# Optimization experiments

Hardware: AMD Instinct MI355X
Metric: run time of the kernel (lower is better)

Reference implementation:

```python
import jax, jax.numpy as jnp
import numpy as np

ECHO_SCALE = 22.8


def setup_inputs() -> dict:
    key = jax.random.key(0)
    k1, k2, k3, k4 = jax.random.split(key, 4)
    n, m = 8192, 4096
    y = jax.random.normal(k1, (n, m), dtype=jnp.float32)
    y_echo = jax.random.normal(k2, (n, m), dtype=jnp.float32)
    f = jax.random.normal(k3, (n, m), dtype=jnp.float32)
    mu = jax.random.uniform(k4, (1,), dtype=jnp.float32)  # scalar threshold in (0,1)
    return {"y": y, "y_echo": y_echo, "f": f, "mu": mu}


def reference(y, y_echo, f, mu):
    n = y.shape[0]
    abs_y = jnp.abs(y)
    # pseudo_l0: hard indicator for |y| >= mu, linear ramp |y|/mu for 0 < |y| < mu
    # (torch precedence: (|y|>=mu) + ((0<|y|<mu) / mu * |y|))
    hard = (abs_y >= mu).astype(y.dtype)
    soft = jnp.logical_and(abs_y > 0, abs_y < mu).astype(y.dtype) / mu * abs_y
    pseudo_l0_loss = jnp.sum(hard + soft) / n
    # l2: trace(|diff| @ |diff|^T) == sum(|diff|**2); same math, no [n,n] matmul
    diff = y_echo / ECHO_SCALE - f
    l2_loss = jnp.sum(jnp.abs(diff) ** 2) / n
    return (pseudo_l0_loss, l2_loss)
```

## Files before the change

### kernel.cpp

```cpp
#include <hip/hip_runtime.h>


#define ECHO_SCALE 22.8f
#define N_ROWS 8192.0f

typedef float fx4 __attribute__((ext_vector_type(4)));

__global__ void init_out_kernel(float* out) {
    if (threadIdx.x < 2) out[threadIdx.x] = 0.0f;
}

__device__ __forceinline__ fx4 ldnt(const fx4* p) {
    return __builtin_nontemporal_load(p);
}

__device__ __forceinline__ void consume(const fx4& vy, const fx4& ve,
                                        const fx4& vf, float inv_mu,
                                        float inv_echo, float& s0, float& s1) {
    s0 += fminf(fabsf(vy.x) * inv_mu, 1.0f);
    s0 += fminf(fabsf(vy.y) * inv_mu, 1.0f);
    s0 += fminf(fabsf(vy.z) * inv_mu, 1.0f);
    s0 += fminf(fabsf(vy.w) * inv_mu, 1.0f);
    float dx = ve.x * inv_echo - vf.x;
    float dy = ve.y * inv_echo - vf.y;
    float dz = ve.z * inv_echo - vf.z;
    float dw = ve.w * inv_echo - vf.w;
    s1 += dx * dx;
    s1 += dy * dy;
    s1 += dz * dz;
    s1 += dw * dw;
}

__global__ __launch_bounds__(256) void loss_kernel(
    const fx4* __restrict__ y,
    const fx4* __restrict__ ye,
    const fx4* __restrict__ f,
    const float* __restrict__ mu_ptr,
    float* __restrict__ out,
    long long n4)
{
    const float mu = mu_ptr[0];
    const float inv_mu = 1.0f / mu;
    const float inv_echo = 1.0f / ECHO_SCALE;

    float s0a = 0.0f, s0b = 0.0f;
    float s1a = 0.0f, s1b = 0.0f;

    const long long per_block = (n4 + gridDim.x - 1) / gridDim.x;
    const long long start = (long long)blockIdx.x * per_block;
    long long end = start + per_block;
    if (end > n4) end = n4;

    const int tid = threadIdx.x;
    const long long bs = blockDim.x;

    long long i = start + tid;
    for (; i + bs < end; i += 2 * bs) {
        fx4 vy0 = ldnt(&y[i]);
        fx4 vy1 = ldnt(&y[i + bs]);
        fx4 ve0 = ldnt(&ye[i]);
        fx4 ve1 = ldnt(&ye[i + bs]);
        fx4 vf0 = ldnt(&f[i]);
        fx4 vf1 = ldnt(&f[i + bs]);
        consume(vy0, ve0, vf0, inv_mu, inv_echo, s0a, s1a);
        consume(vy1, ve1, vf1, inv_mu, inv_echo, s0b, s1b);
    }
    for (; i < end; i += bs) {
        fx4 vy = ldnt(&y[i]);
        fx4 ve = ldnt(&ye[i]);
        fx4 vf = ldnt(&f[i]);
        consume(vy, ve, vf, inv_mu, inv_echo, s0a, s1a);
    }

    float s0 = s0a + s0b;
    float s1 = s1a + s1b;

    #pragma unroll
    for (int off = 32; off > 0; off >>= 1) {
        s0 += __shfl_down(s0, off, 64);
        s1 += __shfl_down(s1, off, 64);
    }

    __shared__ float l0[4];
    __shared__ float l1[4];
    const int wave = threadIdx.x >> 6;
    const int lane = threadIdx.x & 63;
    if (lane == 0) { l0[wave] = s0; l1[wave] = s1; }
    __syncthreads();

    if (threadIdx.x == 0) {
        float t0 = 0.0f, t1 = 0.0f;
        #pragma unroll
        for (int w = 0; w < 4; ++w) { t0 += l0[w]; t1 += l1[w]; }
        atomicAdd(&out[0], t0 * (1.0f / N_ROWS));
        atomicAdd(&out[1], t1 * (1.0f / N_ROWS));
    }
}

extern "C" void kernel_launch(void* const* d_in, const int* in_sizes, int n_in,
                              void* d_out, int out_size, void* d_ws, size_t ws_size,
                              hipStream_t stream) {
    const fx4* y  = (const fx4*)d_in[0];
    const fx4* ye = (const fx4*)d_in[1];
    const fx4* f  = (const fx4*)d_in[2];
    const float* mu  = (const float*)d_in[3];
    float* out = (float*)d_out;

    const long long n  = (long long)in_sizes[0];
    const long long n4 = n / 4;

    init_out_kernel<<<1, 64, 0, stream>>>(out);

    const int block = 256;
    int grid = 2048;
    long long needed = (n4 + block - 1) / block;
    if (needed < grid) grid = (int)needed;

    loss_kernel<<<grid, block, 0, stream>>>(y, ye, f, mu, out, n4);
}
```

Before: 92.77 us.

## Split loss reduction into separate y and echo/f block groups

```diff
diff --git a/kernel.cpp b/kernel.cpp
--- a/kernel.cpp
+++ b/kernel.cpp
@@ -3,6 +3,8 @@
 
 #define ECHO_SCALE 22.8f
 #define N_ROWS 8192.0f
+#define NY_BLOCKS 1024
+#define NEF_BLOCKS 2048
 
 typedef float fx4 __attribute__((ext_vector_type(4)));
 
@@ -14,24 +16,22 @@
     return __builtin_nontemporal_load(p);
 }
 
-__device__ __forceinline__ void consume(const fx4& vy, const fx4& ve,
-                                        const fx4& vf, float inv_mu,
-                                        float inv_echo, float& s0, float& s1) {
-    s0 += fminf(fabsf(vy.x) * inv_mu, 1.0f);
-    s0 += fminf(fabsf(vy.y) * inv_mu, 1.0f);
-    s0 += fminf(fabsf(vy.z) * inv_mu, 1.0f);
-    s0 += fminf(fabsf(vy.w) * inv_mu, 1.0f);
-    float dx = ve.x * inv_echo - vf.x;
-    float dy = ve.y * inv_echo - vf.y;
-    float dz = ve.z * inv_echo - vf.z;
-    float dw = ve.w * inv_echo - vf.w;
-    s1 += dx * dx;
-    s1 += dy * dy;
-    s1 += dz * dz;
-    s1 += dw * dw;
+__device__ __forceinline__ float pl0_4(const fx4& v, float inv_mu) {
+    return fminf(fabsf(v.x) * inv_mu, 1.0f)
+         + fminf(fabsf(v.y) * inv_mu, 1.0f)
+         + fminf(fabsf(v.z) * inv_mu, 1.0f)
+         + fminf(fabsf(v.w) * inv_mu, 1.0f);
 }
 
-__global__ __launch_bounds__(256) void loss_kernel(
+__device__ __forceinline__ float l2_4(const fx4& e, const fx4& ff, float inv_echo) {
+    float dx = e.x * inv_echo - ff.x;
+    float dy = e.y * inv_echo - ff.y;
+    float dz = e.z * inv_echo - ff.z;
+    float dw = e.w * inv_echo - ff.w;
+    return dx * dx + dy * dy + dz * dz + dw * dw;
+}
+
+__global__ __launch_bounds__(256) void loss_split_kernel(
     const fx4* __restrict__ y,
     const fx4* __restrict__ ye,
     const fx4* __restrict__ f,
@@ -39,61 +39,65 @@
     float* __restrict__ out,
     long long n4)
 {
-    const float mu = mu_ptr[0];
-    const float inv_mu = 1.0f / mu;
-    const float inv_echo = 1.0f / ECHO_SCALE;
+    __shared__ float lred[4];
+    const int bid = blockIdx.x;
+    const int tid = threadIdx.x;
+    const long long bs = 256;
 
-    float s0a = 0.0f, s0b = 0.0f;
-    float s1a = 0.0f, s1b = 0.0f;
+    float s = 0.0f;
+    int out_idx;
 
-    const long long per_block = (n4 + gridDim.x - 1) / gridDim.x;
-    const long long start = (long long)blockIdx.x * per_block;
-    long long end = start + per_block;
-    if (end > n4) end = n4;
+    if (bid < NY_BLOCKS) {
+        out_idx = 0;
+        const float inv_mu = 1.0f / mu_ptr[0];
+        const long long pb = (n4 + NY_BLOCKS - 1) / NY_BLOCKS;
+        const long long start = (long long)bid * pb;
+        long long end = start + pb; if (end > n4) end = n4;
 
-    const int tid = threadIdx.x;
-    const long long bs = blockDim.x;
+        float sa = 0.0f, sb = 0.0f;
+        long long i = start + tid;
+        for (; i + bs < end; i += 2 * bs) {
+            fx4 v0 = ldnt(&y[i]);
+            fx4 v1 = ldnt(&y[i + bs]);
+            sa += pl0_4(v0, inv_mu);
+            sb += pl0_4(v1, inv_mu);
+        }
+        for (; i < end; i += bs) sa += pl0_4(ldnt(&y[i]), inv_mu);
+        s = sa + sb;
+    } else {
+        out_idx = 1;
+        const float inv_echo = 1.0f / ECHO_SCALE;
+        const int eb = bid - NY_BLOCKS;
+        const long long pb = (n4 + NEF_BLOCKS - 1) / NEF_BLOCKS;
+        const long long start = (long long)eb * pb;
+        long long end = start + pb; if (end > n4) end = n4;
 
-    long long i = start + tid;
-    for (; i + bs < end; i += 2 * bs) {
-        fx4 vy0 = ldnt(&y[i]);
-        fx4 vy1 = ldnt(&y[i + bs]);
-        fx4 ve0 = ldnt(&ye[i]);
-        fx4 ve1 = ldnt(&ye[i + bs]);
-        fx4 vf0 = ldnt(&f[i]);
-        fx4 vf1 = ldnt(&f[i + bs]);
-        consume(vy0, ve0, vf0, inv_mu, inv_echo, s0a, s1a);
-        consume(vy1, ve1, vf1, inv_mu, inv_echo, s0b, s1b);
-    }
-    for (; i < end; i += bs) {
-        fx4 vy = ldnt(&y[i]);
-        fx4 ve = ldnt(&ye[i]);
-        fx4 vf = ldnt(&f[i]);
-        consume(vy, ve, vf, inv_mu, inv_echo, s0a, s1a);
+        float sa = 0.0f, sb = 0.0f;
+        long long i = start + tid;
+        for (; i + bs < end; i += 2 * bs) {
+            fx4 e0 = ldnt(&ye[i]);
+            fx4 e1 = ldnt(&ye[i + bs]);
+            fx4 f0 = ldnt(&f[i]);
+            fx4 f1 = ldnt(&f[i + bs]);
+            sa += l2_4(e0, f0, inv_echo);
+            sb += l2_4(e1, f1, inv_echo);
+        }
+        for (; i < end; i += bs) sa += l2_4(ldnt(&ye[i]), ldnt(&f[i]), inv_echo);
+        s = sa + sb;
     }
 
-    float s0 = s0a + s0b;
-    float s1 = s1a + s1b;
+    #pragma unroll
+    for (int off = 32; off > 0; off >>= 1)
+        s += __shfl_down(s, off, 64);
 
-    #pragma unroll
-    for (int off = 32; off > 0; off >>= 1) {
-        s0 += __shfl_down(s0, off, 64);
-        s1 += __shfl_down(s1, off, 64);
-    }
-
-    __shared__ float l0[4];
-    __shared__ float l1[4];
-    const int wave = threadIdx.x >> 6;
-    const int lane = threadIdx.x & 63;
-    if (lane == 0) { l0[wave] = s0; l1[wave] = s1; }
+    const int wave = tid >> 6;
+    const int lane = tid & 63;
+    if (lane == 0) lred[wave] = s;
     __syncthreads();
 
-    if (threadIdx.x == 0) {
-        float t0 = 0.0f, t1 = 0.0f;
-        #pragma unroll
-        for (int w = 0; w < 4; ++w) { t0 += l0[w]; t1 += l1[w]; }
-        atomicAdd(&out[0], t0 * (1.0f / N_ROWS));
-        atomicAdd(&out[1], t1 * (1.0f / N_ROWS));
+    if (tid == 0) {
+        float t = (lred[0] + lred[1]) + (lred[2] + lred[3]);
+        atomicAdd(&out[out_idx], t * (1.0f / N_ROWS));
     }
 }
 
@@ -111,10 +115,6 @@
 
     init_out_kernel<<<1, 64, 0, stream>>>(out);
 
-    const int block = 256;
-    int grid = 2048;
-    long long needed = (n4 + block - 1) / block;
-    if (needed < grid) grid = (int)needed;
-
-    loss_kernel<<<grid, block, 0, stream>>>(y, ye, f, mu, out, n4);
+    loss_split_kernel<<<NY_BLOCKS + NEF_BLOCKS, 256, 0, stream>>>(
+        y, ye, f, mu, out, n4);
 }
```

New measurement: 87.46 us. 5.7% less time.
